# Kernel optimization log

Measured on AMD Instinct MI355X. Metric: run time of the kernel, lower is better.

## Reference

```python
import jax, jax.numpy as jnp
import numpy as np

S, B, HID = 2048, 1, 2048
NH, HD = 16, 128  # heads, head_dim (kv_channels); NH*HD == HID
EPS = 1e-5


def setup_inputs() -> dict:
    key = jax.random.key(0)
    ks = jax.random.split(key, 5)
    sc_h = 1.0 / np.sqrt(HID)
    return {
        "hidden_states": jax.random.normal(ks[0], (S, B, HID), jnp.float32),
        "ln_weight": jnp.ones((HID,), jnp.float32),
        "ln_bias": jnp.zeros((HID,), jnp.float32),
        "qkv_weight": jax.random.normal(ks[1], (3 * HID, HID), jnp.float32) * sc_h,
        "qkv_bias": jax.random.normal(ks[2], (3 * HID,), jnp.float32) * 0.02,
        "proj_weight": jax.random.normal(ks[3], (HID, HID), jnp.float32) * sc_h,
        "proj_bias": jax.random.normal(ks[4], (HID,), jnp.float32) * 0.02,
    }


def reference(hidden_states, ln_weight, ln_bias, qkv_weight, qkv_bias, proj_weight, proj_bias):
    s, b, hid = hidden_states.shape
    # LayerNormLinear: LN over last dim, then fused QKV projection
    mu = jnp.mean(hidden_states, axis=-1, keepdims=True)
    var = jnp.mean(jnp.square(hidden_states - mu), axis=-1, keepdims=True)
    ln_x = (hidden_states - mu) * jax.lax.rsqrt(var + EPS) * ln_weight + ln_bias
    mixed = jnp.einsum('sbh,oh->sbo', ln_x, qkv_weight) + qkv_bias  # [S,B,3*HID]
    # fuse_qkv_params=False -> non-interleaved: reshape to [S,B,3*NH,HD], split on dim -2
    mixed = mixed.reshape(s, b, 3 * NH, HD)
    q, k, v = jnp.split(mixed, 3, axis=2)  # each [S,B,NH,HD]
    # scaled dot-product attention with causal mask
    scale = 1.0 / np.sqrt(HD)
    scores = jnp.einsum('sbhd,tbhd->bhst', q, k) * scale  # [B,NH,S,S]
    causal = jnp.tril(jnp.ones((s, s), bool))
    scores = jnp.where(causal, scores, -jnp.inf)
    probs = jax.nn.softmax(scores, axis=-1)
    ctx = jnp.einsum('bhst,tbhd->sbhd', probs, v).reshape(s, b, hid)
    # output projection
    out = jnp.einsum('sbh,oh->sbo', ctx, proj_weight) + proj_bias
    return out
```

## Files before the change

kernel.cpp:

```cpp
#include <hip/hip_runtime.h>
#include <stdint.h>

#define S_LEN 2048
#define HID   2048
#define NHEAD 16
#define HDIM  128
#define LDQK  4096

typedef unsigned short ushort_t;
using bf16x8 = __attribute__((ext_vector_type(8))) short;
using f32x4  = __attribute__((ext_vector_type(4))) float;

__device__ __forceinline__ float bf2f(ushort_t u) {
  union { uint32_t i; float f; } v; v.i = ((uint32_t)u) << 16; return v.f;
}
__device__ __forceinline__ ushort_t f2bf(float f) {
  union { float f; uint32_t i; } v; v.f = f;
  uint32_t r = v.i + 0x7fffu + ((v.i >> 16) & 1u);
  return (ushort_t)(r >> 16);
}
__device__ __forceinline__ void store_val(ushort_t* C, size_t idx, float v) { C[idx] = f2bf(v); }
__device__ __forceinline__ void store_val(float* C, size_t idx, float v) { C[idx] = v; }

__device__ __forceinline__ bf16x8 load8(const ushort_t* p) { return *(const bf16x8*)p; }
__device__ __forceinline__ bf16x8 load8(const float* p) {
  float4 a = *(const float4*)p, b = *(const float4*)(p + 4);
  ushort_t o[8] = { f2bf(a.x), f2bf(a.y), f2bf(a.z), f2bf(a.w),
                    f2bf(b.x), f2bf(b.y), f2bf(b.z), f2bf(b.w) };
  return *(const bf16x8*)o;
}

__device__ __forceinline__ void gl_lds16(const ushort_t* g, short* l) {
  __builtin_amdgcn_global_load_lds((const __attribute__((address_space(1))) void*)g,
                                   (__attribute__((address_space(3))) void*)l, 16, 0, 0);
}

__global__ __launch_bounds__(256) void cvt_f32_bf16(const float* __restrict__ src,
                                                    ushort_t* __restrict__ dst, int n8) {
  int i = blockIdx.x * 256 + threadIdx.x;
  if (i >= n8) return;
  float4 a = ((const float4*)src)[i * 2], b = ((const float4*)src)[i * 2 + 1];
  ushort_t o[8] = { f2bf(a.x), f2bf(a.y), f2bf(a.z), f2bf(a.w),
                    f2bf(b.x), f2bf(b.y), f2bf(b.z), f2bf(b.w) };
  ((uint4*)dst)[i] = *(const uint4*)o;
}

__global__ __launch_bounds__(256) void ln_kernel(const float* __restrict__ x,
                                                 const float* __restrict__ w,
                                                 const float* __restrict__ b,
                                                 ushort_t* __restrict__ y) {
  const int row = blockIdx.x;
  const int t = threadIdx.x;
  const float4* xr = (const float4*)(x + (size_t)row * HID);
  float4 v0 = xr[t], v1 = xr[t + 256];
  float s  = v0.x + v0.y + v0.z + v0.w + v1.x + v1.y + v1.z + v1.w;
  float ss = v0.x*v0.x + v0.y*v0.y + v0.z*v0.z + v0.w*v0.w
           + v1.x*v1.x + v1.y*v1.y + v1.z*v1.z + v1.w*v1.w;
#pragma unroll
  for (int off = 32; off > 0; off >>= 1) { s += __shfl_xor(s, off, 64); ss += __shfl_xor(ss, off, 64); }
  __shared__ float red[8];
  const int wv = t >> 6;
  if ((t & 63) == 0) { red[wv * 2] = s; red[wv * 2 + 1] = ss; }
  __syncthreads();
  s  = red[0] + red[2] + red[4] + red[6];
  ss = red[1] + red[3] + red[5] + red[7];
  const float mu   = s * (1.f / HID);
  const float var  = ss * (1.f / HID) - mu * mu;
  const float rstd = rsqrtf(var + 1e-5f);
  const float4* wr = (const float4*)w;
  const float4* br = (const float4*)b;
  float4 w0 = wr[t], w1 = wr[t + 256];
  float4 b0 = br[t], b1 = br[t + 256];
  ushort_t* yr = y + (size_t)row * HID;
  ushort_t o0[4] = { f2bf((v0.x - mu) * rstd * w0.x + b0.x), f2bf((v0.y - mu) * rstd * w0.y + b0.y),
                     f2bf((v0.z - mu) * rstd * w0.z + b0.z), f2bf((v0.w - mu) * rstd * w0.w + b0.w) };
  ushort_t o1[4] = { f2bf((v1.x - mu) * rstd * w1.x + b1.x), f2bf((v1.y - mu) * rstd * w1.y + b1.y),
                     f2bf((v1.z - mu) * rstd * w1.z + b1.z), f2bf((v1.w - mu) * rstd * w1.w + b1.w) };
  *(uint2*)(&yr[4 * t])         = *(const uint2*)o0;
  *(uint2*)(&yr[4 * (t + 256)]) = *(const uint2*)o1;
}

template <bool SPLIT, typename OUT_T>
__global__ __launch_bounds__(256, 3) void gemm_lds(const ushort_t* __restrict__ A,
                                                   const ushort_t* __restrict__ B,
                                                   const float* __restrict__ bias,
                                                   OUT_T* __restrict__ C,
                                                   ushort_t* __restrict__ VTg,
                                                   int M, int N, int K, int ldc) {
  __shared__ __align__(16) short As[128 * 32];
  __shared__ __align__(16) short Bs[128 * 32];
  const int mb = blockIdx.x * 128, nb = blockIdx.y * 128;
  const int t = threadIdx.x, wave = t >> 6, lane = t & 63;
  const int wm = (wave >> 1) * 64, wn = (wave & 1) * 64;
  const int lrow = lane & 15, quad = lane >> 4;
  const int srow = lane >> 2, scol = (lane & 3) * 8;
  const f32x4 vzero = {0.f, 0.f, 0.f, 0.f};

  f32x4 acc[4][4];
#pragma unroll
  for (int i = 0; i < 4; i++)
#pragma unroll
    for (int j = 0; j < 4; j++) acc[i][j] = vzero;

  for (int k0 = 0; k0 < K; k0 += 32) {
    __syncthreads();
#pragma unroll
    for (int kb = 0; kb < 2; kb++) {
      const int c = wave * 2 + kb;
      const int row = c * 16 + srow;
      gl_lds16(&A[(size_t)(mb + row) * K + k0 + scol], &As[c * 512]);
      gl_lds16(&B[(size_t)(nb + row) * K + k0 + scol], &Bs[c * 512]);
    }
    __syncthreads();
    bf16x8 af[4], bfg[4];
#pragma unroll
    for (int mi = 0; mi < 4; mi++) af[mi] = *(const bf16x8*)(&As[(wm + mi * 16 + lrow) * 32 + quad * 8]);
#pragma unroll
    for (int ni = 0; ni < 4; ni++) bfg[ni] = *(const bf16x8*)(&Bs[(wn + ni * 16 + lrow) * 32 + quad * 8]);
#pragma unroll
    for (int mi = 0; mi < 4; mi++)
#pragma unroll
      for (int ni = 0; ni < 4; ni++)
        acc[mi][ni] = __builtin_amdgcn_mfma_f32_16x16x32_bf16(af[mi], bfg[ni], acc[mi][ni], 0, 0, 0);
  }

#pragma unroll
  for (int mi = 0; mi < 4; mi++)
#pragma unroll
    for (int ni = 0; ni < 4; ni++) {
      const int col = nb + wn + ni * 16 + lrow;
      const float bv = bias[col];
      const int row0 = mb + wm + mi * 16 + quad * 4;
      if (SPLIT && col >= 4096) {
        ushort_t o4[4];
#pragma unroll
        for (int r = 0; r < 4; r++) o4[r] = f2bf(acc[mi][ni][r] + bv);
        *(uint2*)(&VTg[(size_t)(col - 4096) * S_LEN + row0]) = *(const uint2*)o4;
      } else {
#pragma unroll
        for (int r = 0; r < 4; r++)
          store_val(C, (size_t)(row0 + r) * ldc + col, acc[mi][ni][r] + bv);
      }
    }
}

template <bool SPLIT, typename OUT_T, typename BT>
__global__ __launch_bounds__(256, 3) void gemm_bt(const ushort_t* __restrict__ A,
                                                  const BT* __restrict__ B,
                                                  const float* __restrict__ bias,
                                                  OUT_T* __restrict__ C,
                                                  ushort_t* __restrict__ VTg,
                                                  int M, int N, int K, int ldc) {
  __shared__ __align__(16) short As[128 * 40];
  __shared__ __align__(16) short Bs[128 * 40];
  const int mb = blockIdx.x * 128, nb = blockIdx.y * 128;
  const int t = threadIdx.x, wave = t >> 6, lane = t & 63;
  const int wm = (wave >> 1) * 64, wn = (wave & 1) * 64;
  const int lrow = lane & 15, quad = lane >> 4;
  const f32x4 vzero = {0.f, 0.f, 0.f, 0.f};
  f32x4 acc[4][4];
#pragma unroll
  for (int i = 0; i < 4; i++)
#pragma unroll
    for (int j = 0; j < 4; j++) acc[i][j] = vzero;
  for (int k0 = 0; k0 < K; k0 += 32) {
    __syncthreads();
#pragma unroll
    for (int i = 0; i < 2; i++) {
      int c = t + 256 * i;
      int r = c >> 2, kc = (c & 3) * 8;
      *(bf16x8*)(&As[r * 40 + kc]) = load8(&A[(size_t)(mb + r) * K + k0 + kc]);
      *(bf16x8*)(&Bs[r * 40 + kc]) = load8(&B[(size_t)(nb + r) * K + k0 + kc]);
    }
    __syncthreads();
    bf16x8 af[4], bfg[4];
#pragma unroll
    for (int mi = 0; mi < 4; mi++) af[mi] = *(const bf16x8*)(&As[(wm + mi * 16 + lrow) * 40 + quad * 8]);
#pragma unroll
    for (int ni = 0; ni < 4; ni++) bfg[ni] = *(const bf16x8*)(&Bs[(wn + ni * 16 + lrow) * 40 + quad * 8]);
#pragma unroll
    for (int mi = 0; mi < 4; mi++)
#pragma unroll
      for (int ni = 0; ni < 4; ni++)
        acc[mi][ni] = __builtin_amdgcn_mfma_f32_16x16x32_bf16(af[mi], bfg[ni], acc[mi][ni], 0, 0, 0);
  }
#pragma unroll
  for (int mi = 0; mi < 4; mi++)
#pragma unroll
    for (int ni = 0; ni < 4; ni++) {
      const int col = nb + wn + ni * 16 + lrow;
      const float bv = bias[col];
      const int row0 = mb + wm + mi * 16 + quad * 4;
      if (SPLIT && col >= 4096) {
        ushort_t o4[4];
#pragma unroll
        for (int r = 0; r < 4; r++) o4[r] = f2bf(acc[mi][ni][r] + bv);
        *(uint2*)(&VTg[(size_t)(col - 4096) * S_LEN + row0]) = *(const uint2*)o4;
      } else {
#pragma unroll
        for (int r = 0; r < 4; r++)
          store_val(C, (size_t)(row0 + r) * ldc + col, acc[mi][ni][r] + bv);
      }
    }
}

__global__ __launch_bounds__(256, 2) void attn_kernel(const ushort_t* __restrict__ mixedQK,
                                                      const ushort_t* __restrict__ vtg,
                                                      ushort_t* __restrict__ ctx) {
  const int b = blockIdx.x;
  const int h = b & 15;
  const int p = b >> 4;
  const int t = threadIdx.x;
  const int wave = t >> 6, lane = t & 63;
  const int lrow = lane & 15, quad = lane >> 4;
  const float scale = 0.08838834764831845f;
  const float SHIFT = 8.0f;

  __shared__ __align__(16) short Ks[2][64 * 128];
  __shared__ __align__(16) short VTs[2][128 * 64];
  __shared__ __align__(16) short Ps[4][16 * 72];

  const int krow_off = wave * 4 + (lane >> 4);
  const int kgrp = (lane & 15) ^ krow_off;
  const int vrow_off = wave * 8 + (lane >> 3);
  const int vgrp = (lane & 7) ^ (lane >> 3);
  const ushort_t* Kbase = mixedQK + 2048 + h * HDIM;
  const ushort_t* Vbase = vtg + (size_t)h * HDIM * S_LEN;

  const f32x4 vzero = {0.f, 0.f, 0.f, 0.f};
  int cur = 0;

#pragma unroll
  for (int i = 0; i < 4; i++)
    gl_lds16(Kbase + (size_t)(i * 16 + krow_off) * LDQK + kgrp * 8,
             &Ks[cur][(i * 256 + wave * 64) * 8]);
#pragma unroll
  for (int i = 0; i < 4; i++)
    gl_lds16(Vbase + (size_t)(i * 32 + vrow_off) * S_LEN + vgrp * 8,
             &VTs[cur][(i * 256 + wave * 64) * 8]);

  for (int item = 0; item < 2; ++item) {
    const int qblk = item ? (31 - p) : p;
    const int ntiles = qblk + 1;
    const int q0 = qblk * 64 + wave * 16;

    bf16x8 qf[4];
    {
      const ushort_t* Qb = mixedQK + (size_t)(q0 + lrow) * LDQK + h * HDIM;
#pragma unroll
      for (int c = 0; c < 4; c++) qf[c] = *(const bf16x8*)(Qb + c * 32 + quad * 8);
    }

    float lsum[4] = {0.f, 0.f, 0.f, 0.f};
    f32x4 acc[8];
#pragma unroll
    for (int d = 0; d < 8; d++) acc[d] = vzero;

    for (int tk = 0; tk < ntiles; ++tk) {
      const int kv0 = tk * 64;
      __syncthreads();

      const int nv0 = (tk + 1 < ntiles) ? (tk + 1) * 64 : (item == 0 ? 0 : -1);
      if (nv0 >= 0) {
#pragma unroll
        for (int i = 0; i < 4; i++)
          gl_lds16(Kbase + (size_t)(nv0 + i * 16 + krow_off) * LDQK + kgrp * 8,
                   &Ks[cur ^ 1][(i * 256 + wave * 64) * 8]);
#pragma unroll
        for (int i = 0; i < 4; i++)
          gl_lds16(Vbase + (size_t)(i * 32 + vrow_off) * S_LEN + nv0 + vgrp * 8,
                   &VTs[cur ^ 1][(i * 256 + wave * 64) * 8]);
      }

      const short* Kc = Ks[cur];
      const short* Vc = VTs[cur];

      f32x4 sc[4];
#pragma unroll
      for (int ni = 0; ni < 4; ni++) sc[ni] = vzero;
#pragma unroll
      for (int ni = 0; ni < 4; ni++)
#pragma unroll
        for (int c = 0; c < 4; c++) {
          bf16x8 kf = *(const bf16x8*)(&Kc[(((ni * 16 + lrow) << 4) + ((c * 4 + quad) ^ lrow)) * 8]);
          sc[ni] = __builtin_amdgcn_mfma_f32_16x16x32_bf16(qf[c], kf, sc[ni], 0, 0, 0);
        }

      short* P = &Ps[wave][0];
#pragma unroll
      for (int r = 0; r < 4; r++) {
        const int row = q0 + quad * 4 + r;
#pragma unroll
        for (int ni = 0; ni < 4; ni++) {
          const int col = kv0 + ni * 16 + lrow;
          float pe = (col > row) ? 0.f : __expf(sc[ni][r] * scale - SHIFT);
          lsum[r] += pe;
          P[(quad * 4 + r) * 72 + ni * 16 + lrow] = (short)f2bf(pe);
        }
      }

      bf16x8 pf[2];
#pragma unroll
      for (int c = 0; c < 2; c++) pf[c] = *(const bf16x8*)(&P[lrow * 72 + c * 32 + quad * 8]);
#pragma unroll
      for (int d = 0; d < 8; d++)
#pragma unroll
        for (int c = 0; c < 2; c++) {
          bf16x8 vf = *(const bf16x8*)(&Vc[(((d * 16 + lrow) << 3) + ((c * 4 + quad) ^ (lrow & 7))) * 8]);
          acc[d] = __builtin_amdgcn_mfma_f32_16x16x32_bf16(pf[c], vf, acc[d], 0, 0, 0);
        }

      cur ^= 1;
    }

    float inv_l[4];
#pragma unroll
    for (int r = 0; r < 4; r++) {
      float l = lsum[r];
#pragma unroll
      for (int off = 1; off < 16; off <<= 1) l += __shfl_xor(l, off, 16);
      inv_l[r] = 1.f / l;
    }
#pragma unroll
    for (int d = 0; d < 8; d++)
#pragma unroll
      for (int r = 0; r < 4; r++) {
        const int row = q0 + quad * 4 + r;
        ctx[(size_t)row * HID + h * HDIM + d * 16 + lrow] = f2bf(acc[d][r] * inv_l[r]);
      }
  }
}

extern "C" void kernel_launch(void* const* d_in, const int* in_sizes, int n_in,
                              void* d_out, int out_size, void* d_ws, size_t ws_size,
                              hipStream_t stream) {
  const float* hidden = (const float*)d_in[0];
  const float* lnw    = (const float*)d_in[1];
  const float* lnb    = (const float*)d_in[2];
  const float* qkvw   = (const float*)d_in[3];
  const float* qkvb   = (const float*)d_in[4];
  const float* projw  = (const float*)d_in[5];
  const float* projb  = (const float*)d_in[6];
  float* out = (float*)d_out;

  char* ws = (char*)d_ws;
  ushort_t* ln_x    = (ushort_t*)ws;
  ushort_t* mixedQK = (ushort_t*)(ws + ((size_t)8 << 20));
  ushort_t* vtg     = (ushort_t*)(ws + ((size_t)24 << 20));
  ushort_t* qkvw_bf = (ushort_t*)(ws + ((size_t)32 << 20));
  ushort_t* projw_bf= (ushort_t*)(ws + ((size_t)56 << 20));
  ushort_t* ctxb    = ln_x;
  const bool big = ws_size >= ((size_t)64 << 20);

  ln_kernel<<<S_LEN, 256, 0, stream>>>(hidden, lnw, lnb, ln_x);
  if (big) {
    cvt_f32_bf16<<<6144, 256, 0, stream>>>(qkvw, qkvw_bf, 3 * HID * HID / 8);
    cvt_f32_bf16<<<2048, 256, 0, stream>>>(projw, projw_bf, HID * HID / 8);
    gemm_lds<true, ushort_t><<<dim3(16, 48), 256, 0, stream>>>(
        ln_x, qkvw_bf, qkvb, mixedQK, vtg, S_LEN, 3 * HID, HID, LDQK);
  } else {
    gemm_bt<true, ushort_t, float><<<dim3(16, 48), 256, 0, stream>>>(
        ln_x, qkvw, qkvb, mixedQK, vtg, S_LEN, 3 * HID, HID, LDQK);
  }
  attn_kernel<<<256, 256, 0, stream>>>(mixedQK, vtg, ctxb);
  if (big) {
    gemm_lds<false, float><<<dim3(16, 16), 256, 0, stream>>>(
        ctxb, projw_bf, projb, out, nullptr, S_LEN, HID, HID, HID);
  } else {
    gemm_bt<false, float, float><<<dim3(16, 16), 256, 0, stream>>>(
        ctxb, projw, projb, out, nullptr, S_LEN, HID, HID, HID);
  }
}
```

Measured before the change: 277.5 us.

## Double-buffer LDS tiles in GEMM and use 64-row tiles for output projection

The LDS-staged GEMM now uses two shared-memory buffers, so the global-to-LDS copy of the next K slice is issued before the current slice's MFMAs and one barrier per iteration is dropped. The kernel is templated on the M tile size, and the output projection switches to 64-row tiles with twice as many blocks to fill more CUs on the 2048x2048 GEMM. The cost is doubled LDS use per block, which may lower occupancy, and the projection now reuses less of the weight tile per block.

New measurement: 273.7 us. No clear change (-1.4%).

```diff
diff --git a/kernel.cpp b/kernel.cpp
--- a/kernel.cpp
+++ b/kernel.cpp
@@ -80,52 +80,62 @@
   *(uint2*)(&yr[4 * (t + 256)]) = *(const uint2*)o1;
 }
 
-template <bool SPLIT, typename OUT_T>
+template <int MT, bool SPLIT, typename OUT_T>
 __global__ __launch_bounds__(256, 3) void gemm_lds(const ushort_t* __restrict__ A,
                                                    const ushort_t* __restrict__ B,
                                                    const float* __restrict__ bias,
                                                    OUT_T* __restrict__ C,
                                                    ushort_t* __restrict__ VTg,
                                                    int M, int N, int K, int ldc) {
-  __shared__ __align__(16) short As[128 * 32];
-  __shared__ __align__(16) short Bs[128 * 32];
-  const int mb = blockIdx.x * 128, nb = blockIdx.y * 128;
+  constexpr int MI = MT / 32;
+  __shared__ __align__(16) short As[2][MT * 32];
+  __shared__ __align__(16) short Bs[2][128 * 32];
+  const int mb = blockIdx.x * MT, nb = blockIdx.y * 128;
   const int t = threadIdx.x, wave = t >> 6, lane = t & 63;
-  const int wm = (wave >> 1) * 64, wn = (wave & 1) * 64;
+  const int wm = (wave >> 1) * (MT / 2), wn = (wave & 1) * 64;
   const int lrow = lane & 15, quad = lane >> 4;
   const int srow = lane >> 2, scol = (lane & 3) * 8;
   const f32x4 vzero = {0.f, 0.f, 0.f, 0.f};
 
-  f32x4 acc[4][4];
-#pragma unroll
-  for (int i = 0; i < 4; i++)
+  f32x4 acc[MI][4];
+#pragma unroll
+  for (int i = 0; i < MI; i++)
 #pragma unroll
     for (int j = 0; j < 4; j++) acc[i][j] = vzero;
 
+  auto stage = [&](int k0, int buf) {
+#pragma unroll
+    for (int kb = 0; kb < MT / 64; kb++) {
+      const int c = wave * (MT / 64) + kb;
+      gl_lds16(&A[(size_t)(mb + c * 16 + srow) * K + k0 + scol], &As[buf][c * 512]);
+    }
+#pragma unroll
+    for (int kb = 0; kb < 2; kb++) {
+      const int c = wave * 2 + kb;
+      gl_lds16(&B[(size_t)(nb + c * 16 + srow) * K + k0 + scol], &Bs[buf][c * 512]);
+    }
+  };
+
+  stage(0, 0);
+  int cur = 0;
   for (int k0 = 0; k0 < K; k0 += 32) {
     __syncthreads();
-#pragma unroll
-    for (int kb = 0; kb < 2; kb++) {
-      const int c = wave * 2 + kb;
-      const int row = c * 16 + srow;
-      gl_lds16(&A[(size_t)(mb + row) * K + k0 + scol], &As[c * 512]);
-      gl_lds16(&B[(size_t)(nb + row) * K + k0 + scol], &Bs[c * 512]);
-    }
-    __syncthreads();
-    bf16x8 af[4], bfg[4];
-#pragma unroll
-    for (int mi = 0; mi < 4; mi++) af[mi] = *(const bf16x8*)(&As[(wm + mi * 16 + lrow) * 32 + quad * 8]);
-#pragma unroll
-    for (int ni = 0; ni < 4; ni++) bfg[ni] = *(const bf16x8*)(&Bs[(wn + ni * 16 + lrow) * 32 + quad * 8]);
-#pragma unroll
-    for (int mi = 0; mi < 4; mi++)
+    if (k0 + 32 < K) stage(k0 + 32, cur ^ 1);
+    bf16x8 af[MI], bfg[4];
+#pragma unroll
+    for (int mi = 0; mi < MI; mi++) af[mi] = *(const bf16x8*)(&As[cur][(wm + mi * 16 + lrow) * 32 + quad * 8]);
+#pragma unroll
+    for (int ni = 0; ni < 4; ni++) bfg[ni] = *(const bf16x8*)(&Bs[cur][(wn + ni * 16 + lrow) * 32 + quad * 8]);
+#pragma unroll
+    for (int mi = 0; mi < MI; mi++)
 #pragma unroll
       for (int ni = 0; ni < 4; ni++)
         acc[mi][ni] = __builtin_amdgcn_mfma_f32_16x16x32_bf16(af[mi], bfg[ni], acc[mi][ni], 0, 0, 0);
-  }
-
-#pragma unroll
-  for (int mi = 0; mi < 4; mi++)
+    cur ^= 1;
+  }
+
+#pragma unroll
+  for (int mi = 0; mi < MI; mi++)
 #pragma unroll
     for (int ni = 0; ni < 4; ni++) {
       const int col = nb + wn + ni * 16 + lrow;
@@ -356,7 +366,7 @@
   if (big) {
     cvt_f32_bf16<<<6144, 256, 0, stream>>>(qkvw, qkvw_bf, 3 * HID * HID / 8);
     cvt_f32_bf16<<<2048, 256, 0, stream>>>(projw, projw_bf, HID * HID / 8);
-    gemm_lds<true, ushort_t><<<dim3(16, 48), 256, 0, stream>>>(
+    gemm_lds<128, true, ushort_t><<<dim3(16, 48), 256, 0, stream>>>(
         ln_x, qkvw_bf, qkvb, mixedQK, vtg, S_LEN, 3 * HID, HID, LDQK);
   } else {
     gemm_bt<true, ushort_t, float><<<dim3(16, 48), 256, 0, stream>>>(
@@ -364,7 +374,7 @@
   }
   attn_kernel<<<256, 256, 0, stream>>>(mixedQK, vtg, ctxb);
   if (big) {
-    gemm_lds<false, float><<<dim3(16, 16), 256, 0, stream>>>(
+    gemm_lds<64, false, float><<<dim3(32, 16), 256, 0, stream>>>(
         ctxb, projw_bf, projb, out, nullptr, S_LEN, HID, HID, HID);
   } else {
     gemm_bt<false, float, float><<<dim3(16, 16), 256, 0, stream>>>(
```
